# Kernel tuning notes

Measured on AMD Instinct MI355X. Metric: run time of the kernel, lower is better.

## Reference

```python
import jax, jax.numpy as jnp
import numpy as np

N_NODES = 100000
N_EDGES = 1600000
D_IN, D_HID, D_OUT = 64, 64, 40


def setup_inputs() -> dict:
    key = jax.random.key(0)
    ks = jax.random.split(key, 6)
    x = jax.random.normal(ks[0], (N_NODES, D_IN), dtype=jnp.float32)
    edge_index = jax.random.randint(ks[1], (2, N_EDGES), 0, N_NODES, dtype=jnp.int32)
    # Glorot-ish init for the two GCNConv linear weights
    W1 = jax.random.normal(ks[2], (D_IN, D_HID), dtype=jnp.float32) * (1.0 / np.sqrt(D_IN))
    b1 = jnp.zeros((D_HID,), dtype=jnp.float32)
    W2 = jax.random.normal(ks[3], (D_HID, D_OUT), dtype=jnp.float32) * (1.0 / np.sqrt(D_HID))
    b2 = jnp.zeros((D_OUT,), dtype=jnp.float32)
    return {"x": x, "edge_index": edge_index, "W1": W1, "b1": b1, "W2": W2, "b2": b2}


def reference(x, edge_index, W1, b1, W2, b2):
    N = x.shape[0]
    # GCNConv: add self-loops, symmetric normalization D^{-1/2}(A+I)D^{-1/2}
    loops = jnp.arange(N, dtype=edge_index.dtype)
    row = jnp.concatenate([edge_index[0], loops])  # source nodes (messages gathered here)
    col = jnp.concatenate([edge_index[1], loops])  # target nodes (scatter-add here)
    deg = jax.ops.segment_sum(jnp.ones_like(col, dtype=x.dtype), col, num_segments=N)
    dinv = jnp.where(deg > 0, jax.lax.rsqrt(deg), 0.0)
    norm = dinv[row] * dinv[col]  # [E+N]

    def gcn_conv(h, W, b):
        h = h @ W                                   # [N, d_out]
        msg = h[row] * norm[:, None]                # gather + scale  [E+N, d_out]
        return jax.ops.segment_sum(msg, col, num_segments=N) + b

    h = jax.nn.relu(gcn_conv(x, W1, b1))  # dropout is identity in eval mode
    logits = gcn_conv(h, W2, b2)
    return jax.nn.log_softmax(logits, axis=1)
```

## Files before the change

kernel.cpp:

```cpp
#include <hip/hip_runtime.h>
#include <hip/hip_bf16.h>
#include <math.h>

#define N_NODES 100000
#define N_EDGES 1600000
#define D_IN 64
#define D_HID 64
#define D_OUT 40
#define NBUCK 256
#define BSZ 391
#define BCAP 10240
#define P3_EPB 4096
#define P3_GRID ((N_EDGES + P3_EPB - 1) / P3_EPB)
#define GEMM_GRID ((N_NODES + 63) / 64)

typedef __hip_bfloat16 bf16;
typedef __attribute__((ext_vector_type(8))) short short8;
typedef __attribute__((ext_vector_type(4))) float f32x4;

__device__ __forceinline__ float bflo(unsigned int u) {
    union { unsigned int i; float f; } c; c.i = u << 16; return c.f;
}
__device__ __forceinline__ float bfhi(unsigned int u) {
    union { unsigned int i; float f; } c; c.i = u & 0xFFFF0000u; return c.f;
}
__device__ __forceinline__ unsigned short f2b(float f) {
    union { float f; unsigned int u; } c; c.f = f;
    unsigned int u = c.u + 0x7FFFu + ((c.u >> 16) & 1u);
    return (unsigned short)(u >> 16);
}

__global__ __launch_bounds__(256) void k_zero(int* __restrict__ p, int n) {
    int i = blockIdx.x * 256 + threadIdx.x;
    if (i < n) p[i] = 0;
}

__global__ __launch_bounds__(256) void k_cnt(const int* __restrict__ col,
                                             int* __restrict__ bcnt_p) {
    __shared__ int hist[NBUCK];
    hist[threadIdx.x] = 0;
    __syncthreads();
    for (int e = blockIdx.x * 256 + threadIdx.x; e < N_EDGES; e += 256 * 256) {
        unsigned int c = (unsigned int)col[e];
        atomicAdd(&hist[c / 391u], 1);
    }
    __syncthreads();
    int hv = hist[threadIdx.x];
    if (hv) atomicAdd(&bcnt_p[threadIdx.x * 16], hv);
}

__global__ __launch_bounds__(256) void k_scan256(const int* __restrict__ bcnt_p,
                                                 int* __restrict__ fill_p,
                                                 int* __restrict__ bucket_base) {
    __shared__ int sm[256];
    int t = threadIdx.x;
    int v = bcnt_p[t * 16];
    sm[t] = v;
    __syncthreads();
    for (int off = 1; off < 256; off <<= 1) {
        int u = (t >= off) ? sm[t - off] : 0;
        __syncthreads();
        sm[t] += u;
        __syncthreads();
    }
    int excl = sm[t] - v;
    bucket_base[t] = excl;
    fill_p[t * 16] = excl;
    if (t == 255) bucket_base[256] = sm[255];
}

__global__ __launch_bounds__(256) void k_place(const int* __restrict__ ei,
                                               int* __restrict__ fill_p,
                                               int* __restrict__ part) {
    __shared__ int cnt_l[NBUCK];
    __shared__ int base_l[NBUCK];
    cnt_l[threadIdx.x] = 0;
    __syncthreads();
    int e0 = blockIdx.x * P3_EPB;
    unsigned int meta[16];
#pragma unroll
    for (int k = 0; k < 16; k++) {
        int e = e0 + k * 256 + threadIdx.x;
        if (e < N_EDGES) {
            unsigned int c = (unsigned int)ei[N_EDGES + e];
            unsigned int b = c / 391u;
            unsigned int lc = c - b * 391u;
            unsigned int slot = atomicAdd(&cnt_l[b], 1);
            meta[k] = (b << 21) | (lc << 12) | slot;
        } else meta[k] = 0xFFFFFFFFu;
    }
    __syncthreads();
    int cv = cnt_l[threadIdx.x];
    if (cv) base_l[threadIdx.x] = atomicAdd(&fill_p[threadIdx.x * 16], cv);
    __syncthreads();
#pragma unroll
    for (int k = 0; k < 16; k++) {
        if (meta[k] != 0xFFFFFFFFu) {
            int e = e0 + k * 256 + threadIdx.x;
            unsigned int b = meta[k] >> 21;
            unsigned int lc = (meta[k] >> 12) & 0x1FFu;
            unsigned int slot = meta[k] & 0xFFFu;
            unsigned int r = (unsigned int)ei[e];
            part[base_l[b] + slot] = (int)((lc << 17) | r);
        }
    }
}

__global__ __launch_bounds__(256) void k_build(const int* __restrict__ part,
                                               const int* __restrict__ bucket_base,
                                               int* __restrict__ start,
                                               int* __restrict__ nkv,
                                               float* __restrict__ dinv,
                                               int* __restrict__ csr) {
    __shared__ int deg_l[392];
    __shared__ int excl_l[392];
    int tid = threadIdx.x;
    int b = blockIdx.x;
    int base = bucket_base[b], end = bucket_base[b + 1];
    int m = end - base;
    int cbase = b * BCAP;
    for (int i = tid; i < 392; i += 256) deg_l[i] = 0;
    __syncthreads();
    for (int i = tid; i < m; i += 256)
        atomicAdd(&deg_l[(unsigned int)part[base + i] >> 17], 1);
    __syncthreads();
    if (tid < 64) {
        int carry = 0;
        for (int ch = 0; ch < 7; ch++) {
            int idx = ch * 64 + tid;
            int val = (idx < 392) ? ((deg_l[idx] + 7) & ~7) : 0;
            int incl = val;
#pragma unroll
            for (int off = 1; off < 64; off <<= 1) {
                int u = __shfl_up(incl, off, 64);
                if (tid >= off) incl += u;
            }
            if (idx < 392) excl_l[idx] = carry + incl - val;
            carry += __shfl(incl, 63, 64);
        }
    }
    __syncthreads();
    int v0 = b * BSZ;
    for (int vl = tid; vl < BSZ; vl += 256) {
        int v = v0 + vl;
        if (v < N_NODES) {
            int d = deg_l[vl];
            start[v] = cbase + excl_l[vl];
            nkv[v] = (d + 7) >> 3;
            dinv[v] = rsqrtf((float)d + 1.0f);
        }
    }
    __syncthreads();
    for (int j = tid; j < 392 * 8; j += 256) {
        int vl = j >> 3, sl = j & 7;
        int d = deg_l[vl];
        int pc = ((d + 7) & ~7) - d;
        if (sl < pc) csr[cbase + excl_l[vl] + d + sl] = N_NODES;
    }
    __syncthreads();
    for (int i = tid; i < 392; i += 256) deg_l[i] = 0;
    __syncthreads();
    for (int i = tid; i < m; i += 256) {
        unsigned int p = (unsigned int)part[base + i];
        unsigned int lc = p >> 17;
        int s = atomicAdd(&deg_l[lc], 1);
        csr[cbase + excl_l[lc] + s] = (int)(p & 0x1FFFFu);
    }
}

__global__ __launch_bounds__(256) void k_prep(const float* __restrict__ W1,
                                              const float* __restrict__ W2,
                                              unsigned short* __restrict__ wp1,
                                              unsigned short* __restrict__ wp2,
                                              unsigned short* __restrict__ gbz,
                                              unsigned short* __restrict__ g2z) {
    int tid = threadIdx.x;
    if (tid < 64) gbz[(size_t)N_NODES * 64 + tid] = 0;
    if (tid >= 64 && tid < 104) g2z[(size_t)N_NODES * 40 + (tid - 64)] = 0;
    for (int i = tid; i < 4096; i += 256) {
        int e = i & 7, lane = (i >> 3) & 63, t = i >> 9;
        int kk = t >> 2, jt = t & 3;
        int row = kk * 32 + (lane >> 4) * 8 + e;
        int col = jt * 16 + (lane & 15);
        wp1[i] = f2b(W1[row * 64 + col]);
    }
    for (int i = tid; i < 3072; i += 256) {
        int e = i & 7, lane = (i >> 3) & 63, t = i >> 9;
        int kk = t / 3, jt = t - kk * 3;
        int row = kk * 32 + (lane >> 4) * 8 + e;
        int col = jt * 16 + (lane & 15);
        wp2[i] = (col < 40) ? f2b(W2[row * 40 + col]) : (unsigned short)0;
    }
}

__global__ __launch_bounds__(256) void k_gemm1m(const float* __restrict__ x,
                                                const short8* __restrict__ wp,
                                                const float* __restrict__ dinv,
                                                unsigned short* __restrict__ gb) {
    int lane = threadIdx.x & 63;
    int wid = threadIdx.x >> 6;
    int node0 = (blockIdx.x * 4 + wid) * 16;
    if (node0 >= N_NODES) return;
    int vr = node0 + (lane & 15);
    if (vr >= N_NODES) vr = N_NODES - 1;
    int kg = lane >> 4;
    const float* px = x + (size_t)vr * 64 + kg * 8;
    short8 b0, b1;
    {
        float4 f0 = *(const float4*)px;
        float4 f1 = *(const float4*)(px + 4);
        b0[0] = (short)f2b(f0.x); b0[1] = (short)f2b(f0.y);
        b0[2] = (short)f2b(f0.z); b0[3] = (short)f2b(f0.w);
        b0[4] = (short)f2b(f1.x); b0[5] = (short)f2b(f1.y);
        b0[6] = (short)f2b(f1.z); b0[7] = (short)f2b(f1.w);
        float4 g0 = *(const float4*)(px + 32);
        float4 g1 = *(const float4*)(px + 36);
        b1[0] = (short)f2b(g0.x); b1[1] = (short)f2b(g0.y);
        b1[2] = (short)f2b(g0.z); b1[3] = (short)f2b(g0.w);
        b1[4] = (short)f2b(g1.x); b1[5] = (short)f2b(g1.y);
        b1[6] = (short)f2b(g1.z); b1[7] = (short)f2b(g1.w);
    }
    f32x4 acc[4];
#pragma unroll
    for (int jt = 0; jt < 4; jt++) acc[jt] = (f32x4){0.f, 0.f, 0.f, 0.f};
#pragma unroll
    for (int jt = 0; jt < 4; jt++) {
        acc[jt] = __builtin_amdgcn_mfma_f32_16x16x32_bf16(
            wp[(0 * 4 + jt) * 64 + lane], b0, acc[jt], 0, 0, 0);
        acc[jt] = __builtin_amdgcn_mfma_f32_16x16x32_bf16(
            wp[(1 * 4 + jt) * 64 + lane], b1, acc[jt], 0, 0, 0);
    }
    float d = dinv[vr];
    unsigned short* gp = gb + (size_t)vr * 64 + kg * 4;
#pragma unroll
    for (int jt = 0; jt < 4; jt++) {
        unsigned int lo = (unsigned int)f2b(acc[jt][0] * d) |
                          ((unsigned int)f2b(acc[jt][1] * d) << 16);
        unsigned int hi = (unsigned int)f2b(acc[jt][2] * d) |
                          ((unsigned int)f2b(acc[jt][3] * d) << 16);
        *(uint2*)(gp + jt * 16) = make_uint2(lo, hi);
    }
}

__global__ __launch_bounds__(256) void k_gemm2m(const unsigned short* __restrict__ hb,
                                                const short8* __restrict__ wp,
                                                const float* __restrict__ dinv,
                                                unsigned short* __restrict__ g2) {
    int lane = threadIdx.x & 63;
    int wid = threadIdx.x >> 6;
    int node0 = (blockIdx.x * 4 + wid) * 16;
    if (node0 >= N_NODES) return;
    int vr = node0 + (lane & 15);
    if (vr >= N_NODES) vr = N_NODES - 1;
    int kg = lane >> 4;
    const short8* h8 = (const short8*)hb;
    short8 b0 = h8[(size_t)vr * 8 + kg];
    short8 b1 = h8[(size_t)vr * 8 + 4 + kg];
    f32x4 acc[3];
#pragma unroll
    for (int jt = 0; jt < 3; jt++) acc[jt] = (f32x4){0.f, 0.f, 0.f, 0.f};
#pragma unroll
    for (int jt = 0; jt < 3; jt++) {
        acc[jt] = __builtin_amdgcn_mfma_f32_16x16x32_bf16(
            wp[(0 * 3 + jt) * 64 + lane], b0, acc[jt], 0, 0, 0);
        acc[jt] = __builtin_amdgcn_mfma_f32_16x16x32_bf16(
            wp[(1 * 3 + jt) * 64 + lane], b1, acc[jt], 0, 0, 0);
    }
    float d = dinv[vr];
    unsigned short* gp = g2 + (size_t)vr * 40 + kg * 4;
#pragma unroll
    for (int jt = 0; jt < 3; jt++) {
        if (jt == 2 && kg >= 2) break;
        unsigned int lo = (unsigned int)f2b(acc[jt][0] * d) |
                          ((unsigned int)f2b(acc[jt][1] * d) << 16);
        unsigned int hi = (unsigned int)f2b(acc[jt][2] * d) |
                          ((unsigned int)f2b(acc[jt][3] * d) << 16);
        *(uint2*)(gp + jt * 16) = make_uint2(lo, hi);
    }
}

__global__ __launch_bounds__(256) void k_agg1(const int* __restrict__ csr,
                                              const int* __restrict__ start,
                                              const int* __restrict__ nkv,
                                              const unsigned int* __restrict__ gb2,
                                              const float* __restrict__ dinv,
                                              const float* __restrict__ b1,
                                              unsigned short* __restrict__ hb) {
    int lane = threadIdx.x & 63;
    int g = lane >> 3;
    int lq = lane & 7;
    int v = blockIdx.x * 4 + (threadIdx.x >> 6);
    int s = start[v] + g;
    int nk = nkv[v];
    float a0=0.f,a1=0.f,a2=0.f,a3=0.f,a4=0.f,a5=0.f,a6=0.f,a7=0.f;
    if (g == 0) {
        uint4 u = *(const uint4*)(gb2 + (size_t)v * 32 + lq * 4);
        a0 += bflo(u.x); a1 += bfhi(u.x); a2 += bflo(u.y); a3 += bfhi(u.y);
        a4 += bflo(u.z); a5 += bfhi(u.z); a6 += bflo(u.w); a7 += bfhi(u.w);
    }
#pragma unroll 2
    for (int k = 0; k < nk; k++) {
        int r = csr[s + k * 8];
        uint4 u = *(const uint4*)(gb2 + (size_t)r * 32 + lq * 4);
        a0 += bflo(u.x); a1 += bfhi(u.x); a2 += bflo(u.y); a3 += bfhi(u.y);
        a4 += bflo(u.z); a5 += bfhi(u.z); a6 += bflo(u.w); a7 += bfhi(u.w);
    }
#pragma unroll
    for (int o = 8; o < 64; o <<= 1) {
        a0 += __shfl_xor(a0, o, 64); a1 += __shfl_xor(a1, o, 64);
        a2 += __shfl_xor(a2, o, 64); a3 += __shfl_xor(a3, o, 64);
        a4 += __shfl_xor(a4, o, 64); a5 += __shfl_xor(a5, o, 64);
        a6 += __shfl_xor(a6, o, 64); a7 += __shfl_xor(a7, o, 64);
    }
    float d = dinv[v];
    float4 bb0 = ((const float4*)b1)[lq * 2];
    float4 bb1 = ((const float4*)b1)[lq * 2 + 1];
    float h0 = fmaxf(d * a0 + bb0.x, 0.f), h1 = fmaxf(d * a1 + bb0.y, 0.f);
    float h2 = fmaxf(d * a2 + bb0.z, 0.f), h3 = fmaxf(d * a3 + bb0.w, 0.f);
    float h4 = fmaxf(d * a4 + bb1.x, 0.f), h5 = fmaxf(d * a5 + bb1.y, 0.f);
    float h6 = fmaxf(d * a6 + bb1.z, 0.f), h7 = fmaxf(d * a7 + bb1.w, 0.f);
    if (g == 0) {
        uint4 o;
        o.x = (unsigned int)f2b(h0) | ((unsigned int)f2b(h1) << 16);
        o.y = (unsigned int)f2b(h2) | ((unsigned int)f2b(h3) << 16);
        o.z = (unsigned int)f2b(h4) | ((unsigned int)f2b(h5) << 16);
        o.w = (unsigned int)f2b(h6) | ((unsigned int)f2b(h7) << 16);
        *(uint4*)(hb + (size_t)v * 64 + lq * 8) = o;
    }
}

__global__ __launch_bounds__(256) void k_agg2(const int* __restrict__ csr,
                                              const int* __restrict__ start,
                                              const int* __restrict__ nkv,
                                              const unsigned int* __restrict__ g2b2,
                                              const float* __restrict__ dinv,
                                              const float* __restrict__ b2v,
                                              float* __restrict__ out) {
    int lane = threadIdx.x & 63;
    int g = lane >> 3;
    int lq = lane & 7;
    int v = blockIdx.x * 4 + (threadIdx.x >> 6);
    int s = start[v] + g;
    int nk = nkv[v];
    bool act = (lq < 5);
    int lqc = act ? lq : 0;
    float a0=0.f,a1=0.f,a2=0.f,a3=0.f,a4=0.f,a5=0.f,a6=0.f,a7=0.f;
    if (g == 0 && act) {
        uint4 u = *(const uint4*)(g2b2 + (size_t)v * 20 + lq * 4);
        a0 += bflo(u.x); a1 += bfhi(u.x); a2 += bflo(u.y); a3 += bfhi(u.y);
        a4 += bflo(u.z); a5 += bfhi(u.z); a6 += bflo(u.w); a7 += bfhi(u.w);
    }
#pragma unroll 2
    for (int k = 0; k < nk; k++) {
        int r = csr[s + k * 8];
        uint4 u = *(const uint4*)(g2b2 + (size_t)r * 20 + lqc * 4);
        a0 += bflo(u.x); a1 += bfhi(u.x); a2 += bflo(u.y); a3 += bfhi(u.y);
        a4 += bflo(u.z); a5 += bfhi(u.z); a6 += bflo(u.w); a7 += bfhi(u.w);
    }
#pragma unroll
    for (int o = 8; o < 64; o <<= 1) {
        a0 += __shfl_xor(a0, o, 64); a1 += __shfl_xor(a1, o, 64);
        a2 += __shfl_xor(a2, o, 64); a3 += __shfl_xor(a3, o, 64);
        a4 += __shfl_xor(a4, o, 64); a5 += __shfl_xor(a5, o, 64);
        a6 += __shfl_xor(a6, o, 64); a7 += __shfl_xor(a7, o, 64);
    }
    float d = dinv[v];
    float4 bb0 = act ? ((const float4*)b2v)[lq * 2] : make_float4(0.f,0.f,0.f,0.f);
    float4 bb1 = act ? ((const float4*)b2v)[lq * 2 + 1] : make_float4(0.f,0.f,0.f,0.f);
    float l0 = act ? d * a0 + bb0.x : -INFINITY;
    float l1 = act ? d * a1 + bb0.y : -INFINITY;
    float l2 = act ? d * a2 + bb0.z : -INFINITY;
    float l3 = act ? d * a3 + bb0.w : -INFINITY;
    float l4 = act ? d * a4 + bb1.x : -INFINITY;
    float l5 = act ? d * a5 + bb1.y : -INFINITY;
    float l6 = act ? d * a6 + bb1.z : -INFINITY;
    float l7 = act ? d * a7 + bb1.w : -INFINITY;
    float m = fmaxf(fmaxf(fmaxf(l0, l1), fmaxf(l2, l3)),
                    fmaxf(fmaxf(l4, l5), fmaxf(l6, l7)));
#pragma unroll
    for (int o = 1; o < 8; o <<= 1) m = fmaxf(m, __shfl_xor(m, o, 64));
    float ex = act ? (__expf(l0 - m) + __expf(l1 - m) + __expf(l2 - m) +
                      __expf(l3 - m) + __expf(l4 - m) + __expf(l5 - m) +
                      __expf(l6 - m) + __expf(l7 - m)) : 0.f;
#pragma unroll
    for (int o = 1; o < 8; o <<= 1) ex += __shfl_xor(ex, o, 64);
    float lse = m + logf(ex);
    if (g == 0 && act) {
        float* op = out + (size_t)v * 40 + lq * 8;
        *(float4*)op = make_float4(l0 - lse, l1 - lse, l2 - lse, l3 - lse);
        *(float4*)(op + 4) = make_float4(l4 - lse, l5 - lse, l6 - lse, l7 - lse);
    }
}

extern "C" void kernel_launch(void* const* d_in, const int* in_sizes, int n_in,
                              void* d_out, int out_size, void* d_ws, size_t ws_size,
                              hipStream_t stream) {
    const float* x  = (const float*)d_in[0];
    const int*   ei = (const int*)d_in[1];
    const float* W1 = (const float*)d_in[2];
    const float* b1 = (const float*)d_in[3];
    const float* W2 = (const float*)d_in[4];
    const float* b2 = (const float*)d_in[5];
    float* out = (float*)d_out;

    const int N = N_NODES;
    int*   part  = (int*)d_ws;
    int*   csr   = part + N_EDGES;
    int*   start = csr + NBUCK * BCAP;
    int*   nkv   = start + N;
    int*   bcnt  = nkv + N;
    int*   fill  = bcnt + 4096;
    int*   bbase = fill + 4096;
    float* dinv  = (float*)(bbase + 260);
    unsigned short* hb  = (unsigned short*)(dinv + N);
    unsigned short* gb  = hb + (size_t)N * 64;
    unsigned short* g2  = gb + (size_t)(N + 1) * 64;
    unsigned short* wp1 = g2 + (size_t)(N + 1) * 40;
    unsigned short* wp2 = wp1 + 4096;

    k_zero<<<16, 256, 0, stream>>>(bcnt, 4096);
    k_prep<<<1, 256, 0, stream>>>(W1, W2, wp1, wp2, gb, g2);
    k_cnt<<<256, 256, 0, stream>>>(ei + N_EDGES, bcnt);
    k_scan256<<<1, 256, 0, stream>>>(bcnt, fill, bbase);
    k_place<<<P3_GRID, 256, 0, stream>>>(ei, fill, part);
    k_build<<<NBUCK, 256, 0, stream>>>(part, bbase, start, nkv, dinv, csr);
    k_gemm1m<<<GEMM_GRID, 256, 0, stream>>>(x, (const short8*)wp1, dinv, gb);
    k_agg1<<<N / 4, 256, 0, stream>>>(csr, start, nkv, (const unsigned int*)gb,
                                      dinv, b1, hb);
    k_gemm2m<<<GEMM_GRID, 256, 0, stream>>>(hb, (const short8*)wp2, dinv, g2);
    k_agg2<<<N / 4, 256, 0, stream>>>(csr, start, nkv, (const unsigned int*)g2,
                                      dinv, b2, out);
}
```

Baseline: 261.6 us.

## Quantize gathered node features to int8 with per-node scales

Result: faster. 254.3 us (-2.8%).

```diff
diff --git a/kernel.cpp b/kernel.cpp
--- a/kernel.cpp
+++ b/kernel.cpp
@@ -28,6 +28,16 @@
     union { float f; unsigned int u; } c; c.f = f;
     unsigned int u = c.u + 0x7FFFu + ((c.u >> 16) & 1u);
     return (unsigned short)(u >> 16);
+}
+__device__ __forceinline__ float i8f(unsigned int w, int b) {
+    return (float)((int)(w << ((3 - b) * 8)) >> 24);
+}
+__device__ __forceinline__ unsigned int qpack(float v0, float v1, float v2,
+                                              float v3, float qs) {
+    int q0 = __float2int_rn(v0 * qs), q1 = __float2int_rn(v1 * qs);
+    int q2 = __float2int_rn(v2 * qs), q3 = __float2int_rn(v3 * qs);
+    return (unsigned int)(q0 & 255) | ((unsigned int)(q1 & 255) << 8) |
+           ((unsigned int)(q2 & 255) << 16) | ((unsigned int)(q3 & 255) << 24);
 }
 
 __global__ __launch_bounds__(256) void k_zero(int* __restrict__ p, int n) {
@@ -172,11 +182,14 @@
                                               const float* __restrict__ W2,
                                               unsigned short* __restrict__ wp1,
                                               unsigned short* __restrict__ wp2,
-                                              unsigned short* __restrict__ gbz,
-                                              unsigned short* __restrict__ g2z) {
+                                              unsigned int* __restrict__ gb8,
+                                              unsigned int* __restrict__ g2q,
+                                              float* __restrict__ scale1,
+                                              float* __restrict__ scale2) {
     int tid = threadIdx.x;
-    if (tid < 64) gbz[(size_t)N_NODES * 64 + tid] = 0;
-    if (tid >= 64 && tid < 104) g2z[(size_t)N_NODES * 40 + (tid - 64)] = 0;
+    if (tid < 16) gb8[(size_t)N_NODES * 16 + tid] = 0;
+    else if (tid < 32) g2q[(size_t)N_NODES * 16 + (tid - 16)] = 0;
+    else if (tid == 32) { scale1[N_NODES] = 0.f; scale2[N_NODES] = 0.f; }
     for (int i = tid; i < 4096; i += 256) {
         int e = i & 7, lane = (i >> 3) & 63, t = i >> 9;
         int kk = t >> 2, jt = t & 3;
@@ -196,7 +209,8 @@
 __global__ __launch_bounds__(256) void k_gemm1m(const float* __restrict__ x,
                                                 const short8* __restrict__ wp,
                                                 const float* __restrict__ dinv,
-                                                unsigned short* __restrict__ gb) {
+                                                unsigned int* __restrict__ gb8,
+                                                float* __restrict__ scale1) {
     int lane = threadIdx.x & 63;
     int wid = threadIdx.x >> 6;
     int node0 = (blockIdx.x * 4 + wid) * 16;
@@ -231,21 +245,31 @@
             wp[(1 * 4 + jt) * 64 + lane], b1, acc[jt], 0, 0, 0);
     }
     float d = dinv[vr];
-    unsigned short* gp = gb + (size_t)vr * 64 + kg * 4;
-#pragma unroll
-    for (int jt = 0; jt < 4; jt++) {
-        unsigned int lo = (unsigned int)f2b(acc[jt][0] * d) |
-                          ((unsigned int)f2b(acc[jt][1] * d) << 16);
-        unsigned int hi = (unsigned int)f2b(acc[jt][2] * d) |
-                          ((unsigned int)f2b(acc[jt][3] * d) << 16);
-        *(uint2*)(gp + jt * 16) = make_uint2(lo, hi);
-    }
+    float mv[4][4];
+    float amax = 0.f;
+#pragma unroll
+    for (int jt = 0; jt < 4; jt++)
+#pragma unroll
+        for (int i = 0; i < 4; i++) {
+            float val = acc[jt][i] * d;
+            mv[jt][i] = val;
+            amax = fmaxf(amax, fabsf(val));
+        }
+    amax = fmaxf(amax, __shfl_xor(amax, 16, 64));
+    amax = fmaxf(amax, __shfl_xor(amax, 32, 64));
+    float qs = (amax > 0.f) ? 127.f / amax : 0.f;
+    if (kg == 0) scale1[vr] = amax * (1.f / 127.f);
+    unsigned int* gp = gb8 + (size_t)vr * 16 + kg;
+#pragma unroll
+    for (int jt = 0; jt < 4; jt++)
+        gp[jt * 4] = qpack(mv[jt][0], mv[jt][1], mv[jt][2], mv[jt][3], qs);
 }
 
 __global__ __launch_bounds__(256) void k_gemm2m(const unsigned short* __restrict__ hb,
                                                 const short8* __restrict__ wp,
                                                 const float* __restrict__ dinv,
-                                                unsigned short* __restrict__ g2) {
+                                                unsigned int* __restrict__ g2q,
+                                                float* __restrict__ scale2) {
     int lane = threadIdx.x & 63;
     int wid = threadIdx.x >> 6;
     int node0 = (blockIdx.x * 4 + wid) * 16;
@@ -267,22 +291,33 @@
             wp[(1 * 3 + jt) * 64 + lane], b1, acc[jt], 0, 0, 0);
     }
     float d = dinv[vr];
-    unsigned short* gp = g2 + (size_t)vr * 40 + kg * 4;
-#pragma unroll
-    for (int jt = 0; jt < 3; jt++) {
-        if (jt == 2 && kg >= 2) break;
-        unsigned int lo = (unsigned int)f2b(acc[jt][0] * d) |
-                          ((unsigned int)f2b(acc[jt][1] * d) << 16);
-        unsigned int hi = (unsigned int)f2b(acc[jt][2] * d) |
-                          ((unsigned int)f2b(acc[jt][3] * d) << 16);
-        *(uint2*)(gp + jt * 16) = make_uint2(lo, hi);
-    }
+    bool v2 = (kg < 2);
+    float mv[3][4];
+    float amax = 0.f;
+#pragma unroll
+    for (int jt = 0; jt < 3; jt++)
+#pragma unroll
+        for (int i = 0; i < 4; i++) {
+            float val = acc[jt][i] * d;
+            mv[jt][i] = val;
+            if (jt < 2 || v2) amax = fmaxf(amax, fabsf(val));
+        }
+    amax = fmaxf(amax, __shfl_xor(amax, 16, 64));
+    amax = fmaxf(amax, __shfl_xor(amax, 32, 64));
+    float qs = (amax > 0.f) ? 127.f / amax : 0.f;
+    if (kg == 0) scale2[vr] = amax * (1.f / 127.f);
+    unsigned int* gp = g2q + (size_t)vr * 16;
+    gp[0 * 4 + kg] = qpack(mv[0][0], mv[0][1], mv[0][2], mv[0][3], qs);
+    gp[1 * 4 + kg] = qpack(mv[1][0], mv[1][1], mv[1][2], mv[1][3], qs);
+    gp[8 + kg] = v2 ? qpack(mv[2][0], mv[2][1], mv[2][2], mv[2][3], qs) : 0u;
+    gp[12 + kg] = 0u;
 }
 
 __global__ __launch_bounds__(256) void k_agg1(const int* __restrict__ csr,
                                               const int* __restrict__ start,
                                               const int* __restrict__ nkv,
-                                              const unsigned int* __restrict__ gb2,
+                                              const unsigned int* __restrict__ gb8,
+                                              const float* __restrict__ scale1,
                                               const float* __restrict__ dinv,
                                               const float* __restrict__ b1,
                                               unsigned short* __restrict__ hb) {
@@ -294,16 +329,22 @@
     int nk = nkv[v];
     float a0=0.f,a1=0.f,a2=0.f,a3=0.f,a4=0.f,a5=0.f,a6=0.f,a7=0.f;
     if (g == 0) {
-        uint4 u = *(const uint4*)(gb2 + (size_t)v * 32 + lq * 4);
-        a0 += bflo(u.x); a1 += bfhi(u.x); a2 += bflo(u.y); a3 += bfhi(u.y);
-        a4 += bflo(u.z); a5 += bfhi(u.z); a6 += bflo(u.w); a7 += bfhi(u.w);
+        float sc = scale1[v];
+        uint2 u = *(const uint2*)(gb8 + (size_t)v * 16 + lq * 2);
+        a0 = fmaf(i8f(u.x,0), sc, a0); a1 = fmaf(i8f(u.x,1), sc, a1);
+        a2 = fmaf(i8f(u.x,2), sc, a2); a3 = fmaf(i8f(u.x,3), sc, a3);
+        a4 = fmaf(i8f(u.y,0), sc, a4); a5 = fmaf(i8f(u.y,1), sc, a5);
+        a6 = fmaf(i8f(u.y,2), sc, a6); a7 = fmaf(i8f(u.y,3), sc, a7);
     }
 #pragma unroll 2
     for (int k = 0; k < nk; k++) {
         int r = csr[s + k * 8];
-        uint4 u = *(const uint4*)(gb2 + (size_t)r * 32 + lq * 4);
-        a0 += bflo(u.x); a1 += bfhi(u.x); a2 += bflo(u.y); a3 += bfhi(u.y);
-        a4 += bflo(u.z); a5 += bfhi(u.z); a6 += bflo(u.w); a7 += bfhi(u.w);
+        float sc = scale1[r];
+        uint2 u = *(const uint2*)(gb8 + (size_t)r * 16 + lq * 2);
+        a0 = fmaf(i8f(u.x,0), sc, a0); a1 = fmaf(i8f(u.x,1), sc, a1);
+        a2 = fmaf(i8f(u.x,2), sc, a2); a3 = fmaf(i8f(u.x,3), sc, a3);
+        a4 = fmaf(i8f(u.y,0), sc, a4); a5 = fmaf(i8f(u.y,1), sc, a5);
+        a6 = fmaf(i8f(u.y,2), sc, a6); a7 = fmaf(i8f(u.y,3), sc, a7);
     }
 #pragma unroll
     for (int o = 8; o < 64; o <<= 1) {
@@ -332,7 +373,8 @@
 __global__ __launch_bounds__(256) void k_agg2(const int* __restrict__ csr,
                                               const int* __restrict__ start,
                                               const int* __restrict__ nkv,
-                                              const unsigned int* __restrict__ g2b2,
+                                              const unsigned int* __restrict__ g2q,
+                                              const float* __restrict__ scale2,
                                               const float* __restrict__ dinv,
                                               const float* __restrict__ b2v,
                                               float* __restrict__ out) {
@@ -343,19 +385,24 @@
     int s = start[v] + g;
     int nk = nkv[v];
     bool act = (lq < 5);
-    int lqc = act ? lq : 0;
     float a0=0.f,a1=0.f,a2=0.f,a3=0.f,a4=0.f,a5=0.f,a6=0.f,a7=0.f;
-    if (g == 0 && act) {
-        uint4 u = *(const uint4*)(g2b2 + (size_t)v * 20 + lq * 4);
-        a0 += bflo(u.x); a1 += bfhi(u.x); a2 += bflo(u.y); a3 += bfhi(u.y);
-        a4 += bflo(u.z); a5 += bfhi(u.z); a6 += bflo(u.w); a7 += bfhi(u.w);
+    if (g == 0) {
+        float sc = scale2[v];
+        uint2 u = *(const uint2*)(g2q + (size_t)v * 16 + lq * 2);
+        a0 = fmaf(i8f(u.x,0), sc, a0); a1 = fmaf(i8f(u.x,1), sc, a1);
+        a2 = fmaf(i8f(u.x,2), sc, a2); a3 = fmaf(i8f(u.x,3), sc, a3);
+        a4 = fmaf(i8f(u.y,0), sc, a4); a5 = fmaf(i8f(u.y,1), sc, a5);
+        a6 = fmaf(i8f(u.y,2), sc, a6); a7 = fmaf(i8f(u.y,3), sc, a7);
     }
 #pragma unroll 2
     for (int k = 0; k < nk; k++) {
         int r = csr[s + k * 8];
-        uint4 u = *(const uint4*)(g2b2 + (size_t)r * 20 + lqc * 4);
-        a0 += bflo(u.x); a1 += bfhi(u.x); a2 += bflo(u.y); a3 += bfhi(u.y);
-        a4 += bflo(u.z); a5 += bfhi(u.z); a6 += bflo(u.w); a7 += bfhi(u.w);
+        float sc = scale2[r];
+        uint2 u = *(const uint2*)(g2q + (size_t)r * 16 + lq * 2);
+        a0 = fmaf(i8f(u.x,0), sc, a0); a1 = fmaf(i8f(u.x,1), sc, a1);
+        a2 = fmaf(i8f(u.x,2), sc, a2); a3 = fmaf(i8f(u.x,3), sc, a3);
+        a4 = fmaf(i8f(u.y,0), sc, a4); a5 = fmaf(i8f(u.y,1), sc, a5);
+        a6 = fmaf(i8f(u.y,2), sc, a6); a7 = fmaf(i8f(u.y,3), sc, a7);
     }
 #pragma unroll
     for (int o = 8; o < 64; o <<= 1) {
@@ -412,22 +459,22 @@
     int*   fill  = bcnt + 4096;
     int*   bbase = fill + 4096;
     float* dinv  = (float*)(bbase + 260);
-    unsigned short* hb  = (unsigned short*)(dinv + N);
-    unsigned short* gb  = hb + (size_t)N * 64;
-    unsigned short* g2  = gb + (size_t)(N + 1) * 64;
-    unsigned short* wp1 = g2 + (size_t)(N + 1) * 40;
+    float* scale1 = dinv + N;
+    float* scale2 = scale1 + N + 4;
+    unsigned short* hb  = (unsigned short*)(scale2 + N + 4);
+    unsigned int* gb8 = (unsigned int*)(hb + (size_t)N * 64);
+    unsigned int* g2q = gb8 + (size_t)(N + 1) * 16;
+    unsigned short* wp1 = (unsigned short*)(g2q + (size_t)(N + 1) * 16);
     unsigned short* wp2 = wp1 + 4096;
 
     k_zero<<<16, 256, 0, stream>>>(bcnt, 4096);
-    k_prep<<<1, 256, 0, stream>>>(W1, W2, wp1, wp2, gb, g2);
+    k_prep<<<1, 256, 0, stream>>>(W1, W2, wp1, wp2, gb8, g2q, scale1, scale2);
     k_cnt<<<256, 256, 0, stream>>>(ei + N_EDGES, bcnt);
     k_scan256<<<1, 256, 0, stream>>>(bcnt, fill, bbase);
     k_place<<<P3_GRID, 256, 0, stream>>>(ei, fill, part);
     k_build<<<NBUCK, 256, 0, stream>>>(part, bbase, start, nkv, dinv, csr);
-    k_gemm1m<<<GEMM_GRID, 256, 0, stream>>>(x, (const short8*)wp1, dinv, gb);
-    k_agg1<<<N / 4, 256, 0, stream>>>(csr, start, nkv, (const unsigned int*)gb,
-                                      dinv, b1, hb);
-    k_gemm2m<<<GEMM_GRID, 256, 0, stream>>>(hb, (const short8*)wp2, dinv, g2);
-    k_agg2<<<N / 4, 256, 0, stream>>>(csr, start, nkv, (const unsigned int*)g2,
-                                      dinv, b2, out);
-}
+    k_gemm1m<<<GEMM_GRID, 256, 0, stream>>>(x, (const short8*)wp1, dinv, gb8, scale1);
+    k_agg1<<<N / 4, 256, 0, stream>>>(csr, start, nkv, gb8, scale1, dinv, b1, hb);
+    k_gemm2m<<<GEMM_GRID, 256, 0, stream>>>(hb, (const short8*)wp2, dinv, g2q, scale2);
+    k_agg2<<<N / 4, 256, 0, stream>>>(csr, start, nkv, g2q, scale2, dinv, b2, out);
+}
```
